# Kernel optimization log

Hardware: AMD Instinct MI355X
Metric: run time of the kernel (lower is better)

Reference implementation:

```python
import jax, jax.numpy as jnp
import numpy as np

DIM = 768
H = 64
W = 64
NB = 8
BS = DIM // NB
LAMBD = 0.01
SCALE = 0.02


def softshrink(x, lambd):
    return jnp.sign(x) * jnp.maximum(jnp.abs(x) - lambd, 0.0)


def setup_inputs() -> dict:
    key = jax.random.key(0)
    ks = jax.random.split(key, 7)
    x = jax.random.normal(ks[0], (8, H * W, DIM), dtype=jnp.float32)
    w1 = SCALE * jax.random.normal(ks[1], (2, NB, BS, BS), dtype=jnp.float32)
    b1 = SCALE * jax.random.normal(ks[2], (2, NB, BS), dtype=jnp.float32)
    w2 = SCALE * jax.random.normal(ks[3], (2, NB, BS, BS), dtype=jnp.float32)
    b2 = SCALE * jax.random.normal(ks[4], (2, NB, BS), dtype=jnp.float32)
    # Conv1d(dim, dim, kernel_size=1) == per-token linear: weight [C_out, C_in], bias [C_out]
    Wb = (1.0 / np.sqrt(DIM)) * jax.random.normal(ks[5], (DIM, DIM), dtype=jnp.float32)
    bb = (1.0 / np.sqrt(DIM)) * jax.random.normal(ks[6], (DIM,), dtype=jnp.float32)
    return {"x": x, "w1": w1, "b1": b1, "w2": w2, "b2": b2, "Wb": Wb, "bb": bb}


def reference(x, w1, b1, w2, b2, Wb, bb):
    B, N, C = x.shape
    # bias path: Conv1d with kernel 1 is a linear map over channels
    bias = jnp.einsum('bnc,dc->bnd', x, Wb) + bb
    # spectral path
    xg = x.reshape(B, H, W, C)
    xf = jnp.fft.rfft2(xg, axes=(1, 2), norm='ortho')          # [B, H, W//2+1, C] complex64
    xf = xf.reshape(B, H, W // 2 + 1, NB, BS)
    xr, xi = jnp.real(xf), jnp.imag(xf)
    # layer 1: complex block-diagonal matmul + relu
    r1 = jax.nn.relu(jnp.einsum('...bd,bdk->...bk', xr, w1[0])
                     - jnp.einsum('...bd,bdk->...bk', xi, w1[1]) + b1[0])
    i1 = jax.nn.relu(jnp.einsum('...bd,bdk->...bk', xr, w1[1])
                     + jnp.einsum('...bd,bdk->...bk', xi, w1[0]) + b1[1])
    # layer 2
    r2 = (jnp.einsum('...bd,bdk->...bk', r1, w2[0])
          - jnp.einsum('...bd,bdk->...bk', i1, w2[1]) + b2[0])
    i2 = (jnp.einsum('...bd,bdk->...bk', r1, w2[1])
          + jnp.einsum('...bd,bdk->...bk', i1, w2[0]) + b2[1])
    r2 = softshrink(r2, LAMBD)
    i2 = softshrink(i2, LAMBD)
    xc = (r2 + 1j * i2).reshape(B, H, W // 2 + 1, C)
    xo = jnp.fft.irfft2(xc, s=(H, W), axes=(1, 2), norm='ortho')  # [B, H, W, C]
    return xo.reshape(B, N, C) + bias
```

## Files before the change

kernel.cpp:

```cpp
#include <hip/hip_runtime.h>
#include <math.h>

#ifndef M_PI
#define M_PI 3.14159265358979323846
#endif

namespace {

constexpr int kDim = 768;
constexpr int kNKW = 33;
constexpr int kB = 8;
constexpr float kLambd = 0.01f;
constexpr size_t kXFElems = (size_t)kB * kNKW * 64 * kDim;

typedef __attribute__((ext_vector_type(8))) __bf16 bf16x8;
typedef __attribute__((ext_vector_type(8))) short short8;
typedef __attribute__((ext_vector_type(4))) float f32x4;

alignas(16) __device__ unsigned short g_wT[4 * 8 * 96 * 96];
alignas(16) __device__ unsigned short g_twC[64 * 64];
alignas(16) __device__ unsigned short g_twS[64 * 64];
alignas(16) __device__ unsigned short g_iwC[64 * 64];
alignas(16) __device__ unsigned short g_iwS[64 * 64];

__device__ inline unsigned short f2bf(float f) {
  unsigned int u = __float_as_uint(f);
  unsigned int r = (u + 0x7FFFu + ((u >> 16) & 1u)) >> 16;
  return (unsigned short)r;
}

__device__ inline bf16x8 s2b(short8 s) { return __builtin_bit_cast(bf16x8, s); }
__device__ inline bf16x8 negb(short8 s) {
  s ^= (short)0x8000;
  return __builtin_bit_cast(bf16x8, s);
}

__device__ inline void gload_lds16(const void* g, void* l) {
  __builtin_amdgcn_global_load_lds(
      (const __attribute__((address_space(1))) unsigned int*)g,
      (__attribute__((address_space(3))) unsigned int*)l, 16, 0, 0);
}

__global__ __launch_bounds__(256) void init_tables_kernel() {
  const int e = blockIdx.x * 256 + threadIdx.x;
  if (e >= 4096) return;
  const int a = e >> 6;
  const int bcol = e & 63;
  const float ang = (float)(2.0 * M_PI / 64.0) * (float)((a * bcol) & 63);
  float s_, c_;
  __sincosf(ang, &s_, &c_);
  g_twC[e] = f2bf(0.125f * c_);
  g_twS[e] = f2bf(0.125f * s_);
  unsigned short cv = 0, sv = 0;
  if (bcol < 33) {
    const float al = (bcol == 0 || bcol == 32) ? 0.125f : 0.25f;
    cv = f2bf(al * c_);
    sv = f2bf(-al * s_);
  }
  g_iwC[e] = cv;
  g_iwS[e] = sv;
}

__global__ __launch_bounds__(256) void cvt_f32_bf16_kernel(
    const float* __restrict__ in, unsigned short* __restrict__ out, int n4) {
  int i = blockIdx.x * 256 + threadIdx.x;
  if (i >= n4) return;
  const float4 v = reinterpret_cast<const float4*>(in)[i];
  ushort4 o;
  o.x = f2bf(v.x); o.y = f2bf(v.y); o.z = f2bf(v.z); o.w = f2bf(v.w);
  reinterpret_cast<ushort4*>(out)[i] = o;
}

__global__ __launch_bounds__(256) void cvt_w_kernel(
    const float* __restrict__ w1, const float* __restrict__ w2) {
  const int e = blockIdx.x * 256 + threadIdx.x;
  if (e >= 4 * 8 * 96 * 96) return;
  const int k = e % 96;
  const int d = (e / 96) % 96;
  const int nbm = e / 9216;
  const int mtx = nbm >> 3;
  const int nb = nbm & 7;
  const float* src =
      (mtx < 2 ? w1 : w2) + ((size_t)(mtx & 1) * 8 + nb) * 9216;
  g_wT[((size_t)nbm * 96 + k) * 96 + d] = f2bf(src[d * 96 + k]);
}

__global__ __launch_bounds__(256) void mfma_gemm_kernel(
    const unsigned short* __restrict__ xbf, const unsigned short* __restrict__ wbf,
    const float* __restrict__ bb, float* __restrict__ out) {
  __shared__ unsigned short As[128 * 32];
  __shared__ unsigned short Bs[128 * 32];
  const int t = threadIdx.x;
  const int lane = t & 63;
  const int wid = t >> 6;
  const int wm = wid >> 1;
  const int wn = wid & 1;
  const int id = blockIdx.x;
  const int swz = (id & 7) * 192 + (id >> 3);
  const int m0 = (swz / 6) * 128;
  const int n0 = (swz % 6) * 128;

  f32x4 acc[4][4];
#pragma unroll
  for (int i = 0; i < 4; ++i)
#pragma unroll
    for (int j = 0; j < 4; ++j) acc[i][j] = (f32x4){0.f, 0.f, 0.f, 0.f};

  char* AsB = (char*)As;
  char* BsB = (char*)Bs;
  const int cl = lane & 15;
  const int kg = lane >> 4;

  for (int k0 = 0; k0 < 768; k0 += 32) {
#pragma unroll
    for (int i = 0; i < 2; ++i) {
      const int off = (wid * 2 + i) * 1024 + lane * 16;
      const int row = off >> 6;
      const int kb = off & 63;
      const char* gA = (const char*)xbf + ((size_t)(m0 + row) * 768 + k0) * 2 + kb;
      gload_lds16(gA, AsB + (wid * 2 + i) * 1024);
      const char* gB = (const char*)wbf + ((size_t)(n0 + row) * 768 + k0) * 2 + kb;
      gload_lds16(gB, BsB + (wid * 2 + i) * 1024);
    }
    asm volatile("s_waitcnt vmcnt(0)" ::: "memory");
    __syncthreads();

    bf16x8 av[4], bv[4];
#pragma unroll
    for (int mi = 0; mi < 4; ++mi) {
      const int r = wm * 64 + mi * 16 + cl;
      av[mi] = *reinterpret_cast<const bf16x8*>(AsB + r * 64 + kg * 16);
    }
#pragma unroll
    for (int ni = 0; ni < 4; ++ni) {
      const int r = wn * 64 + ni * 16 + cl;
      bv[ni] = *reinterpret_cast<const bf16x8*>(BsB + r * 64 + kg * 16);
    }
#pragma unroll
    for (int mi = 0; mi < 4; ++mi)
#pragma unroll
      for (int ni = 0; ni < 4; ++ni)
        acc[mi][ni] = __builtin_amdgcn_mfma_f32_16x16x32_bf16(
            av[mi], bv[ni], acc[mi][ni], 0, 0, 0);
    __syncthreads();
  }

#pragma unroll
  for (int ni = 0; ni < 4; ++ni) {
    const int n = n0 + wn * 64 + ni * 16 + cl;
    const float bias = bb[n];
#pragma unroll
    for (int mi = 0; mi < 4; ++mi) {
      const int m = m0 + wm * 64 + mi * 16 + kg * 4;
#pragma unroll
      for (int r = 0; r < 4; ++r) {
        out[(size_t)(m + r) * 768 + n] = acc[mi][ni][r] + bias;
      }
    }
  }
}

__global__ __launch_bounds__(256) void rfft_row_mfma_kernel(
    const float* __restrict__ x, unsigned short* __restrict__ xbf,
    unsigned short* __restrict__ XFr, unsigned short* __restrict__ XFi) {
  __shared__ alignas(16) unsigned short xs[64 * 66];
  const int t = threadIdx.x;
  const int lane = t & 63;
  const int wv = t >> 6;
  const int cl = lane & 15;
  const int kg = lane >> 4;
  const int bh = blockIdx.x;
  const int b = bh >> 6;
  const int h = bh & 63;
  const int c0 = blockIdx.y * 64;

  {
    const float* xrow = x + (size_t)bh * (64 * 768) + c0;
    unsigned short* xbrow = xbf + (size_t)bh * (64 * 768) + c0;
#pragma unroll 4
    for (int it = 0; it < 16; ++it) {
      const int w = wv * 16 + it;
      const float v = xrow[(size_t)w * 768 + lane];
      const unsigned short bv = f2bf(v);
      xbrow[(size_t)w * 768 + lane] = bv;
      xs[w * 66 + lane] = bv;
    }
  }
  __syncthreads();

  const int cA = wv * 16 + cl;
  short8 ax[2];
#pragma unroll
  for (int kf = 0; kf < 2; ++kf) {
#pragma unroll
    for (int j = 0; j < 8; ++j)
      ax[kf][j] = (short)xs[(kf * 32 + kg * 8 + j) * 66 + cA];
  }

  f32x4 aR[3], aI[3];
#pragma unroll
  for (int nt = 0; nt < 3; ++nt) {
    aR[nt] = (f32x4){0.f, 0.f, 0.f, 0.f};
    aI[nt] = (f32x4){0.f, 0.f, 0.f, 0.f};
  }

#pragma unroll
  for (int nt = 0; nt < 3; ++nt) {
#pragma unroll
    for (int kf = 0; kf < 2; ++kf) {
      const int row = nt * 16 + cl;
      const int w0 = kf * 32 + kg * 8;
      const short8 cs = *reinterpret_cast<const short8*>(g_twC + row * 64 + w0);
      const short8 ss = *reinterpret_cast<const short8*>(g_twS + row * 64 + w0);
      aR[nt] = __builtin_amdgcn_mfma_f32_16x16x32_bf16(s2b(ax[kf]), s2b(cs), aR[nt], 0, 0, 0);
      aI[nt] = __builtin_amdgcn_mfma_f32_16x16x32_bf16(s2b(ax[kf]), negb(ss), aI[nt], 0, 0, 0);
    }
  }

  const int cD = c0 + wv * 16 + kg * 4;
#pragma unroll
  for (int nt = 0; nt < 3; ++nt) {
    const int kh = nt * 16 + cl;
    if (kh <= 32) {
      const size_t off = (((size_t)b * kNKW + kh) * 64 + h) * 768 + cD;
      ushort4 vr, vi;
      vr.x = f2bf(aR[nt][0]); vr.y = f2bf(aR[nt][1]);
      vr.z = f2bf(aR[nt][2]); vr.w = f2bf(aR[nt][3]);
      vi.x = f2bf(aI[nt][0]); vi.y = f2bf(aI[nt][1]);
      vi.z = f2bf(aI[nt][2]); vi.w = f2bf(aI[nt][3]);
      *reinterpret_cast<ushort4*>(XFr + off) = vr;
      *reinterpret_cast<ushort4*>(XFi + off) = vi;
    }
  }
}

__global__ __launch_bounds__(256) void spectral_mid_kernel(
    unsigned short* __restrict__ Xr, unsigned short* __restrict__ Xi,
    const float* __restrict__ b1, const float* __restrict__ b2) {
  __shared__ alignas(16) unsigned short sXr[64 * 104];
  __shared__ alignas(16) unsigned short sXi[64 * 104];
  __shared__ alignas(16) unsigned short sYr[64 * 104];
  __shared__ alignas(16) unsigned short sYi[64 * 104];
  const int t = threadIdx.x;
  const int lane = t & 63;
  const int wid = t >> 6;
  const int wm = wid >> 1;
  const int wn = wid & 1;
  const int cl = lane & 15;
  const int kg = lane >> 4;
  const int nb = blockIdx.y;
  const size_t gbase = (size_t)blockIdx.x * (64 * 768) + nb * 96;

  {
    const int row = t >> 2;
    const int q = t & 3;
    const size_t gof = gbase + (size_t)row * 768 + q * 24;
    unsigned short* lr = sXr + row * 104 + q * 24;
    unsigned short* li = sXi + row * 104 + q * 24;
#pragma unroll
    for (int v = 0; v < 3; ++v) {
      *reinterpret_cast<short8*>(lr + v * 8) =
          *reinterpret_cast<const short8*>(Xr + gof + v * 8);
      *reinterpret_cast<short8*>(li + v * 8) =
          *reinterpret_cast<const short8*>(Xi + gof + v * 8);
    }
  }
  __syncthreads();

  f32x4 accR[2][3], accI[2][3];

#pragma unroll
  for (int mt = 0; mt < 2; ++mt)
#pragma unroll
    for (int nt = 0; nt < 3; ++nt) {
      accR[mt][nt] = (f32x4){0.f, 0.f, 0.f, 0.f};
      accI[mt][nt] = (f32x4){0.f, 0.f, 0.f, 0.f};
    }
#pragma unroll
  for (int kf = 0; kf < 2; ++kf) {
    const int k0 = kf * 32 + kg * 8;
    short8 bR[3], bI[3];
#pragma unroll
    for (int nt = 0; nt < 3; ++nt) {
      const int col = wn * 48 + nt * 16 + cl;
#pragma unroll
      for (int j = 0; j < 8; ++j) {
        bR[nt][j] = (short)sXr[(k0 + j) * 104 + col];
        bI[nt][j] = (short)sXi[(k0 + j) * 104 + col];
      }
    }
#pragma unroll
    for (int mt = 0; mt < 2; ++mt) {
      const int row = wm * 32 + mt * 16 + cl;
      const short8 cs = *reinterpret_cast<const short8*>(g_twC + row * 64 + k0);
      const short8 ss = *reinterpret_cast<const short8*>(g_twS + row * 64 + k0);
#pragma unroll
      for (int nt = 0; nt < 3; ++nt) {
        accR[mt][nt] = __builtin_amdgcn_mfma_f32_16x16x32_bf16(s2b(cs), s2b(bR[nt]), accR[mt][nt], 0, 0, 0);
        accR[mt][nt] = __builtin_amdgcn_mfma_f32_16x16x32_bf16(s2b(ss), s2b(bI[nt]), accR[mt][nt], 0, 0, 0);
        accI[mt][nt] = __builtin_amdgcn_mfma_f32_16x16x32_bf16(s2b(cs), s2b(bI[nt]), accI[mt][nt], 0, 0, 0);
        accI[mt][nt] = __builtin_amdgcn_mfma_f32_16x16x32_bf16(negb(ss), s2b(bR[nt]), accI[mt][nt], 0, 0, 0);
      }
    }
  }
#pragma unroll
  for (int mt = 0; mt < 2; ++mt) {
#pragma unroll
    for (int nt = 0; nt < 3; ++nt) {
      const int col = wn * 48 + nt * 16 + cl;
      const int row0 = wm * 32 + mt * 16 + kg * 4;
#pragma unroll
      for (int r = 0; r < 4; ++r) {
        sYr[(row0 + r) * 104 + col] = f2bf(accR[mt][nt][r]);
        sYi[(row0 + r) * 104 + col] = f2bf(accI[mt][nt][r]);
      }
    }
  }
  __syncthreads();

  const unsigned short* wt1r = g_wT + (size_t)(0 * 8 + nb) * 9216;
  const unsigned short* wt1i = g_wT + (size_t)(1 * 8 + nb) * 9216;
  const unsigned short* wt2r = g_wT + (size_t)(2 * 8 + nb) * 9216;
  const unsigned short* wt2i = g_wT + (size_t)(3 * 8 + nb) * 9216;

#pragma unroll
  for (int mt = 0; mt < 2; ++mt)
#pragma unroll
    for (int nt = 0; nt < 3; ++nt) {
      accR[mt][nt] = (f32x4){0.f, 0.f, 0.f, 0.f};
      accI[mt][nt] = (f32x4){0.f, 0.f, 0.f, 0.f};
    }
#pragma unroll
  for (int kk = 0; kk < 3; ++kk) {
    const int ko = kk * 32 + kg * 8;
    short8 axr[2], axi[2];
#pragma unroll
    for (int mt = 0; mt < 2; ++mt) {
      const int row = wm * 32 + mt * 16 + cl;
      axr[mt] = *reinterpret_cast<const short8*>(sYr + row * 104 + ko);
      axi[mt] = *reinterpret_cast<const short8*>(sYi + row * 104 + ko);
    }
    short8 wr_[3], wi_[3];
#pragma unroll
    for (int nt = 0; nt < 3; ++nt) {
      const int rw = wn * 48 + nt * 16 + cl;
      wr_[nt] = *reinterpret_cast<const short8*>(wt1r + rw * 96 + ko);
      wi_[nt] = *reinterpret_cast<const short8*>(wt1i + rw * 96 + ko);
    }
#pragma unroll
    for (int mt = 0; mt < 2; ++mt) {
      const bf16x8 ar = s2b(axr[mt]);
      const bf16x8 ai = s2b(axi[mt]);
      const bf16x8 ain = negb(axi[mt]);
#pragma unroll
      for (int nt = 0; nt < 3; ++nt) {
        accR[mt][nt] = __builtin_amdgcn_mfma_f32_16x16x32_bf16(ar, s2b(wr_[nt]), accR[mt][nt], 0, 0, 0);
        accR[mt][nt] = __builtin_amdgcn_mfma_f32_16x16x32_bf16(ain, s2b(wi_[nt]), accR[mt][nt], 0, 0, 0);
        accI[mt][nt] = __builtin_amdgcn_mfma_f32_16x16x32_bf16(ar, s2b(wi_[nt]), accI[mt][nt], 0, 0, 0);
        accI[mt][nt] = __builtin_amdgcn_mfma_f32_16x16x32_bf16(ai, s2b(wr_[nt]), accI[mt][nt], 0, 0, 0);
      }
    }
  }
#pragma unroll
  for (int nt = 0; nt < 3; ++nt) {
    const int col = wn * 48 + nt * 16 + cl;
    const float br = b1[nb * 96 + col];
    const float bi = b1[768 + nb * 96 + col];
#pragma unroll
    for (int mt = 0; mt < 2; ++mt) {
      const int row0 = wm * 32 + mt * 16 + kg * 4;
#pragma unroll
      for (int r = 0; r < 4; ++r) {
        sXr[(row0 + r) * 104 + col] = f2bf(fmaxf(accR[mt][nt][r] + br, 0.f));
        sXi[(row0 + r) * 104 + col] = f2bf(fmaxf(accI[mt][nt][r] + bi, 0.f));
      }
    }
  }
  __syncthreads();

#pragma unroll
  for (int mt = 0; mt < 2; ++mt)
#pragma unroll
    for (int nt = 0; nt < 3; ++nt) {
      accR[mt][nt] = (f32x4){0.f, 0.f, 0.f, 0.f};
      accI[mt][nt] = (f32x4){0.f, 0.f, 0.f, 0.f};
    }
#pragma unroll
  for (int kk = 0; kk < 3; ++kk) {
    const int ko = kk * 32 + kg * 8;
    short8 axr[2], axi[2];
#pragma unroll
    for (int mt = 0; mt < 2; ++mt) {
      const int row = wm * 32 + mt * 16 + cl;
      axr[mt] = *reinterpret_cast<const short8*>(sXr + row * 104 + ko);
      axi[mt] = *reinterpret_cast<const short8*>(sXi + row * 104 + ko);
    }
    short8 wr_[3], wi_[3];
#pragma unroll
    for (int nt = 0; nt < 3; ++nt) {
      const int rw = wn * 48 + nt * 16 + cl;
      wr_[nt] = *reinterpret_cast<const short8*>(wt2r + rw * 96 + ko);
      wi_[nt] = *reinterpret_cast<const short8*>(wt2i + rw * 96 + ko);
    }
#pragma unroll
    for (int mt = 0; mt < 2; ++mt) {
      const bf16x8 ar = s2b(axr[mt]);
      const bf16x8 ai = s2b(axi[mt]);
      const bf16x8 ain = negb(axi[mt]);
#pragma unroll
      for (int nt = 0; nt < 3; ++nt) {
        accR[mt][nt] = __builtin_amdgcn_mfma_f32_16x16x32_bf16(ar, s2b(wr_[nt]), accR[mt][nt], 0, 0, 0);
        accR[mt][nt] = __builtin_amdgcn_mfma_f32_16x16x32_bf16(ain, s2b(wi_[nt]), accR[mt][nt], 0, 0, 0);
        accI[mt][nt] = __builtin_amdgcn_mfma_f32_16x16x32_bf16(ar, s2b(wi_[nt]), accI[mt][nt], 0, 0, 0);
        accI[mt][nt] = __builtin_amdgcn_mfma_f32_16x16x32_bf16(ai, s2b(wr_[nt]), accI[mt][nt], 0, 0, 0);
      }
    }
  }
#pragma unroll
  for (int nt = 0; nt < 3; ++nt) {
    const int col = wn * 48 + nt * 16 + cl;
    const float br = b2[nb * 96 + col];
    const float bi = b2[768 + nb * 96 + col];
#pragma unroll
    for (int mt = 0; mt < 2; ++mt) {
      const int row0 = wm * 32 + mt * 16 + kg * 4;
#pragma unroll
      for (int r = 0; r < 4; ++r) {
        float vr = accR[mt][nt][r] + br;
        float vi = accI[mt][nt][r] + bi;
        vr = (vr > kLambd) ? (vr - kLambd) : ((vr < -kLambd) ? (vr + kLambd) : 0.f);
        vi = (vi > kLambd) ? (vi - kLambd) : ((vi < -kLambd) ? (vi + kLambd) : 0.f);
        sYr[(row0 + r) * 104 + col] = f2bf(vr);
        sYi[(row0 + r) * 104 + col] = f2bf(vi);
      }
    }
  }
  __syncthreads();

#pragma unroll
  for (int mt = 0; mt < 2; ++mt)
#pragma unroll
    for (int nt = 0; nt < 3; ++nt) {
      accR[mt][nt] = (f32x4){0.f, 0.f, 0.f, 0.f};
      accI[mt][nt] = (f32x4){0.f, 0.f, 0.f, 0.f};
    }
#pragma unroll
  for (int kf = 0; kf < 2; ++kf) {
    const int k0 = kf * 32 + kg * 8;
    short8 bR[3], bI[3];
#pragma unroll
    for (int nt = 0; nt < 3; ++nt) {
      const int col = wn * 48 + nt * 16 + cl;
#pragma unroll
      for (int j = 0; j < 8; ++j) {
        bR[nt][j] = (short)sYr[(k0 + j) * 104 + col];
        bI[nt][j] = (short)sYi[(k0 + j) * 104 + col];
      }
    }
#pragma unroll
    for (int mt = 0; mt < 2; ++mt) {
      const int row = wm * 32 + mt * 16 + cl;
      const short8 cs = *reinterpret_cast<const short8*>(g_twC + row * 64 + k0);
      const short8 ss = *reinterpret_cast<const short8*>(g_twS + row * 64 + k0);
#pragma unroll
      for (int nt = 0; nt < 3; ++nt) {
        accR[mt][nt] = __builtin_amdgcn_mfma_f32_16x16x32_bf16(s2b(cs), s2b(bR[nt]), accR[mt][nt], 0, 0, 0);
        accR[mt][nt] = __builtin_amdgcn_mfma_f32_16x16x32_bf16(negb(ss), s2b(bI[nt]), accR[mt][nt], 0, 0, 0);
        accI[mt][nt] = __builtin_amdgcn_mfma_f32_16x16x32_bf16(s2b(cs), s2b(bI[nt]), accI[mt][nt], 0, 0, 0);
        accI[mt][nt] = __builtin_amdgcn_mfma_f32_16x16x32_bf16(s2b(ss), s2b(bR[nt]), accI[mt][nt], 0, 0, 0);
      }
    }
  }
#pragma unroll
  for (int mt = 0; mt < 2; ++mt) {
#pragma unroll
    for (int nt = 0; nt < 3; ++nt) {
      const int col = wn * 48 + nt * 16 + cl;
      const int row0 = wm * 32 + mt * 16 + kg * 4;
#pragma unroll
      for (int r = 0; r < 4; ++r) {
        const size_t off = gbase + (size_t)(row0 + r) * 768 + col;
        Xr[off] = f2bf(accR[mt][nt][r]);
        Xi[off] = f2bf(accI[mt][nt][r]);
      }
    }
  }
}

__global__ __launch_bounds__(256) void irfft_row_add_mfma_kernel(
    const unsigned short* __restrict__ Zr, const unsigned short* __restrict__ Zi,
    float* __restrict__ out) {
  const int t = threadIdx.x;
  const int lane = t & 63;
  const int wv = t >> 6;
  const int cl = lane & 15;
  const int kg = lane >> 4;
  const int bh = blockIdx.x;
  const int b = bh >> 6;
  const int h = bh & 63;
  const int cb = blockIdx.y * 64 + wv * 16;

  const int cA = cb + cl;
  short8 azr[2], azi[2];
#pragma unroll
  for (int kf = 0; kf < 2; ++kf) {
#pragma unroll
    for (int j = 0; j < 8; ++j) {
      const int kw = kf * 32 + kg * 8 + j;
      short zr = 0, zi = 0;
      if (kw < 33) {
        const size_t off = (((size_t)b * kNKW + kw) * 64 + h) * 768 + cA;
        zr = (short)Zr[off];
        zi = (short)Zi[off];
      }
      azr[kf][j] = zr;
      azi[kf][j] = zi;
    }
  }

  const int cD = cb + kg * 4;
  float* obase = out + ((size_t)bh * 64) * 768;
  f32x4 aO[4];
#pragma unroll
  for (int nt = 0; nt < 4; ++nt) {
    const int w = nt * 16 + cl;
    aO[nt] = *reinterpret_cast<const f32x4*>(obase + (size_t)w * 768 + cD);
  }

#pragma unroll
  for (int nt = 0; nt < 4; ++nt) {
#pragma unroll
    for (int kf = 0; kf < 2; ++kf) {
      const int row = nt * 16 + cl;
      const int kw0 = kf * 32 + kg * 8;
      const short8 bc = *reinterpret_cast<const short8*>(g_iwC + row * 64 + kw0);
      const short8 bs = *reinterpret_cast<const short8*>(g_iwS + row * 64 + kw0);
      aO[nt] = __builtin_amdgcn_mfma_f32_16x16x32_bf16(s2b(azr[kf]), s2b(bc), aO[nt], 0, 0, 0);
      aO[nt] = __builtin_amdgcn_mfma_f32_16x16x32_bf16(s2b(azi[kf]), s2b(bs), aO[nt], 0, 0, 0);
    }
  }

#pragma unroll
  for (int nt = 0; nt < 4; ++nt) {
    const int w = nt * 16 + cl;
    *reinterpret_cast<f32x4*>(obase + (size_t)w * 768 + cD) = aO[nt];
  }
}

}

extern "C" void kernel_launch(void* const* d_in, const int* in_sizes, int n_in,
                              void* d_out, int out_size, void* d_ws,
                              size_t ws_size, hipStream_t stream) {
  (void)in_sizes; (void)n_in; (void)out_size;
  const float* x  = (const float*)d_in[0];
  const float* w1 = (const float*)d_in[1];
  const float* b1 = (const float*)d_in[2];
  const float* w2 = (const float*)d_in[3];
  const float* b2 = (const float*)d_in[4];
  const float* Wb = (const float*)d_in[5];
  const float* bb = (const float*)d_in[6];
  float* out = (float*)d_out;

  if (ws_size < 2 * kXFElems * sizeof(float)) return;
  unsigned short* xbf = (unsigned short*)d_ws;
  unsigned short* wbf = xbf + (size_t)32768 * 768;
  unsigned short* XFr = wbf + (size_t)768 * 768;
  unsigned short* XFi = XFr + kXFElems;

  init_tables_kernel<<<dim3(16), 256, 0, stream>>>();
  cvt_f32_bf16_kernel<<<dim3((768 * 768 / 4 + 255) / 256), 256, 0, stream>>>(
      Wb, wbf, 768 * 768 / 4);
  cvt_w_kernel<<<dim3(4 * 8 * 96 * 96 / 256), 256, 0, stream>>>(w1, w2);
  rfft_row_mfma_kernel<<<dim3(512, 12), 256, 0, stream>>>(x, xbf, XFr, XFi);
  mfma_gemm_kernel<<<dim3(1536), 256, 0, stream>>>(xbf, wbf, bb, out);
  spectral_mid_kernel<<<dim3(264, 8), 256, 0, stream>>>(XFr, XFi, b1, b2);
  irfft_row_add_mfma_kernel<<<dim3(512, 12), 256, 0, stream>>>(XFr, XFi, out);
}
```

Baseline: 279.7 us.

## Prefetch twiddle tables into registers and stage rfft output through LDS

Hoists the global twiddle-factor loads (DFT cos/sin tables) to the start of the rfft, spectral-mid and irfft kernels so their latency overlaps with the input loads. In the rfft row kernel, output is first written to shared memory and then stored as contiguous 64-channel rows, replacing scattered 8-byte stores. This is meant to hide load latency and coalesce writes, at the cost of more registers and extra LDS plus a barrier.

Result: no change. 275.3 us (-1.5%).

```diff
diff --git a/kernel.cpp b/kernel.cpp
--- a/kernel.cpp
+++ b/kernel.cpp
@@ -164,6 +164,8 @@
     const float* __restrict__ x, unsigned short* __restrict__ xbf,
     unsigned short* __restrict__ XFr, unsigned short* __restrict__ XFi) {
   __shared__ alignas(16) unsigned short xs[64 * 66];
+  __shared__ alignas(16) unsigned short sOr[33 * 68];
+  __shared__ alignas(16) unsigned short sOi[33 * 68];
   const int t = threadIdx.x;
   const int lane = t & 63;
   const int wv = t >> 6;
@@ -173,6 +175,18 @@
   const int b = bh >> 6;
   const int h = bh & 63;
   const int c0 = blockIdx.y * 64;
+
+  short8 pcs[3][2], pss[3][2];
+#pragma unroll
+  for (int nt = 0; nt < 3; ++nt) {
+#pragma unroll
+    for (int kf = 0; kf < 2; ++kf) {
+      const int row = nt * 16 + cl;
+      const int w0 = kf * 32 + kg * 8;
+      pcs[nt][kf] = *reinterpret_cast<const short8*>(g_twC + row * 64 + w0);
+      pss[nt][kf] = *reinterpret_cast<const short8*>(g_twS + row * 64 + w0);
+    }
+  }
 
   {
     const float* xrow = x + (size_t)bh * (64 * 768) + c0;
@@ -208,29 +222,34 @@
   for (int nt = 0; nt < 3; ++nt) {
 #pragma unroll
     for (int kf = 0; kf < 2; ++kf) {
-      const int row = nt * 16 + cl;
-      const int w0 = kf * 32 + kg * 8;
-      const short8 cs = *reinterpret_cast<const short8*>(g_twC + row * 64 + w0);
-      const short8 ss = *reinterpret_cast<const short8*>(g_twS + row * 64 + w0);
-      aR[nt] = __builtin_amdgcn_mfma_f32_16x16x32_bf16(s2b(ax[kf]), s2b(cs), aR[nt], 0, 0, 0);
-      aI[nt] = __builtin_amdgcn_mfma_f32_16x16x32_bf16(s2b(ax[kf]), negb(ss), aI[nt], 0, 0, 0);
-    }
-  }
-
-  const int cD = c0 + wv * 16 + kg * 4;
+      aR[nt] = __builtin_amdgcn_mfma_f32_16x16x32_bf16(s2b(ax[kf]), s2b(pcs[nt][kf]), aR[nt], 0, 0, 0);
+      aI[nt] = __builtin_amdgcn_mfma_f32_16x16x32_bf16(s2b(ax[kf]), negb(pss[nt][kf]), aI[nt], 0, 0, 0);
+    }
+  }
+
+  const int cL = wv * 16 + kg * 4;
 #pragma unroll
   for (int nt = 0; nt < 3; ++nt) {
     const int kh = nt * 16 + cl;
     if (kh <= 32) {
-      const size_t off = (((size_t)b * kNKW + kh) * 64 + h) * 768 + cD;
       ushort4 vr, vi;
       vr.x = f2bf(aR[nt][0]); vr.y = f2bf(aR[nt][1]);
       vr.z = f2bf(aR[nt][2]); vr.w = f2bf(aR[nt][3]);
       vi.x = f2bf(aI[nt][0]); vi.y = f2bf(aI[nt][1]);
       vi.z = f2bf(aI[nt][2]); vi.w = f2bf(aI[nt][3]);
-      *reinterpret_cast<ushort4*>(XFr + off) = vr;
-      *reinterpret_cast<ushort4*>(XFi + off) = vi;
-    }
+      *reinterpret_cast<ushort4*>(sOr + kh * 68 + cL) = vr;
+      *reinterpret_cast<ushort4*>(sOi + kh * 68 + cL) = vi;
+    }
+  }
+  __syncthreads();
+  for (int idx = t; idx < 33 * 16; idx += 256) {
+    const int row = idx >> 4;
+    const int c4 = (idx & 15) * 4;
+    const size_t off = (((size_t)b * kNKW + row) * 64 + h) * 768 + c0 + c4;
+    *reinterpret_cast<ushort4*>(XFr + off) =
+        *reinterpret_cast<const ushort4*>(sOr + row * 68 + c4);
+    *reinterpret_cast<ushort4*>(XFi + off) =
+        *reinterpret_cast<const ushort4*>(sOi + row * 68 + c4);
   }
 }
 
@@ -251,6 +270,18 @@
   const int nb = blockIdx.y;
   const size_t gbase = (size_t)blockIdx.x * (64 * 768) + nb * 96;
 
+  short8 pcs[2][2], pss[2][2];
+#pragma unroll
+  for (int mt = 0; mt < 2; ++mt) {
+#pragma unroll
+    for (int kf = 0; kf < 2; ++kf) {
+      const int row = wm * 32 + mt * 16 + cl;
+      const int k0 = kf * 32 + kg * 8;
+      pcs[mt][kf] = *reinterpret_cast<const short8*>(g_twC + row * 64 + k0);
+      pss[mt][kf] = *reinterpret_cast<const short8*>(g_twS + row * 64 + k0);
+    }
+  }
+
   {
     const int row = t >> 2;
     const int q = t & 3;
@@ -291,9 +322,8 @@
     }
 #pragma unroll
     for (int mt = 0; mt < 2; ++mt) {
-      const int row = wm * 32 + mt * 16 + cl;
-      const short8 cs = *reinterpret_cast<const short8*>(g_twC + row * 64 + k0);
-      const short8 ss = *reinterpret_cast<const short8*>(g_twS + row * 64 + k0);
+      const short8 cs = pcs[mt][kf];
+      const short8 ss = pss[mt][kf];
 #pragma unroll
       for (int nt = 0; nt < 3; ++nt) {
         accR[mt][nt] = __builtin_amdgcn_mfma_f32_16x16x32_bf16(s2b(cs), s2b(bR[nt]), accR[mt][nt], 0, 0, 0);
@@ -459,9 +489,8 @@
     }
 #pragma unroll
     for (int mt = 0; mt < 2; ++mt) {
-      const int row = wm * 32 + mt * 16 + cl;
-      const short8 cs = *reinterpret_cast<const short8*>(g_twC + row * 64 + k0);
-      const short8 ss = *reinterpret_cast<const short8*>(g_twS + row * 64 + k0);
+      const short8 cs = pcs[mt][kf];
+      const short8 ss = pss[mt][kf];
 #pragma unroll
       for (int nt = 0; nt < 3; ++nt) {
         accR[mt][nt] = __builtin_amdgcn_mfma_f32_16x16x32_bf16(s2b(cs), s2b(bR[nt]), accR[mt][nt], 0, 0, 0);
@@ -500,6 +529,18 @@
   const int h = bh & 63;
   const int cb = blockIdx.y * 64 + wv * 16;
 
+  short8 pbc[4][2], pbs[4][2];
+#pragma unroll
+  for (int nt = 0; nt < 4; ++nt) {
+#pragma unroll
+    for (int kf = 0; kf < 2; ++kf) {
+      const int row = nt * 16 + cl;
+      const int kw0 = kf * 32 + kg * 8;
+      pbc[nt][kf] = *reinterpret_cast<const short8*>(g_iwC + row * 64 + kw0);
+      pbs[nt][kf] = *reinterpret_cast<const short8*>(g_iwS + row * 64 + kw0);
+    }
+  }
+
   const int cA = cb + cl;
   short8 azr[2], azi[2];
 #pragma unroll
@@ -531,12 +572,8 @@
   for (int nt = 0; nt < 4; ++nt) {
 #pragma unroll
     for (int kf = 0; kf < 2; ++kf) {
-      const int row = nt * 16 + cl;
-      const int kw0 = kf * 32 + kg * 8;
-      const short8 bc = *reinterpret_cast<const short8*>(g_iwC + row * 64 + kw0);
-      const short8 bs = *reinterpret_cast<const short8*>(g_iwS + row * 64 + kw0);
-      aO[nt] = __builtin_amdgcn_mfma_f32_16x16x32_bf16(s2b(azr[kf]), s2b(bc), aO[nt], 0, 0, 0);
-      aO[nt] = __builtin_amdgcn_mfma_f32_16x16x32_bf16(s2b(azi[kf]), s2b(bs), aO[nt], 0, 0, 0);
+      aO[nt] = __builtin_amdgcn_mfma_f32_16x16x32_bf16(s2b(azr[kf]), s2b(pbc[nt][kf]), aO[nt], 0, 0, 0);
+      aO[nt] = __builtin_amdgcn_mfma_f32_16x16x32_bf16(s2b(azi[kf]), s2b(pbs[nt][kf]), aO[nt], 0, 0, 0);
     }
   }
 
```
